# Optimization experiments

Hardware: AMD Instinct MI355X
Metric: run time of the kernel (lower is better)

The kernel has to match this reference:

```python
import jax, jax.numpy as jnp
import numpy as np

TAU = 2.0       # LIF time constant
VTH = 1.0       # V_THRESHOLD
ALPHA = 2.0     # ATan surrogate alpha (spikingjelly default)
SCALE = 0.125

@jax.custom_vjp
def spike(x):
    # Heaviside spike with ATan surrogate gradient
    return (x >= 0.0).astype(x.dtype)

def _spike_fwd(x):
    return (x >= 0.0).astype(x.dtype), x

def _spike_bwd(x, g):
    sg = (ALPHA / 2.0) / (1.0 + (jnp.pi / 2.0 * ALPHA * x) ** 2)
    return (g * sg,)

spike.defvjp(_spike_fwd, _spike_bwd)

def lif(x_seq):
    # multi-step LIF: v += (x - v)/tau; spike; hard reset (v_reset=0, detach_reset)
    def step(v, x):
        v = v + (x - v) / TAU
        s = spike(v - VTH)
        v = v * (1.0 - jax.lax.stop_gradient(s))
        return v, s
    _, s = jax.lax.scan(step, jnp.zeros_like(x_seq[0]), x_seq)
    return s

def conn_lif(x_seq, y_seq):
    # connecting LIF: membrane charged by conv output + identity shortcut
    def step(v, xy):
        x, y = xy
        v = v + ((x + y) - v) / TAU
        s = spike(v - VTH)
        v = v * (1.0 - jax.lax.stop_gradient(s))
        return v, s
    _, s = jax.lax.scan(step, jnp.zeros_like(x_seq[0]), (x_seq, y_seq))
    return s

def conv1x1(x, W, b):
    # x: [T,B,C,N]; 1x1 Conv1d == channel GEMM
    return jnp.einsum('tbcn,oc->tbon', x, W) + b[None, None, :, None]

def setup_inputs() -> dict:
    key = jax.random.key(0)
    T, B, C, H, W = 4, 16, 512, 32, 32
    ks = jax.random.split(key, 5)
    wscale = 1.0 / np.sqrt(C)
    inp = {
        'x': jax.random.normal(ks[0], (T, B, C, H, W), jnp.float32),
        'Wq': jax.random.normal(ks[1], (C, C), jnp.float32) * wscale,
        'bq': jnp.zeros((C,), jnp.float32),
        'Wk': jax.random.normal(ks[2], (C, C), jnp.float32) * wscale,
        'bk': jnp.zeros((C,), jnp.float32),
        'Wv': jax.random.normal(ks[3], (C, C), jnp.float32) * wscale,
        'bv': jnp.zeros((C,), jnp.float32),
        'Wp': jax.random.normal(ks[4], (C, C), jnp.float32) * wscale,
        'bp': jnp.zeros((C,), jnp.float32),
        'num_heads': 8,
    }
    return inp

def reference(x, Wq, bq, Wk, bk, Wv, bv, Wp, bp, num_heads):
    T, B, C, H, W = x.shape
    N = H * W
    h = num_heads
    d = C // h
    qkv_x = x.reshape(T, B, C, N)

    def to_heads(s):  # [T,B,C,N] -> [T,B,h,N,d]
        return s.reshape(T, B, h, d, N).transpose(0, 1, 2, 4, 3)

    q = to_heads(lif(conv1x1(qkv_x, Wq, bq)))
    k = to_heads(lif(conv1x1(qkv_x, Wk, bk)))
    v = to_heads(lif(conv1x1(qkv_x, Wv, bv)))

    kv = jnp.einsum('tbhnd,tbhne->tbhde', k, v)            # K^T V: [T,B,h,d,d]
    out = jnp.einsum('tbhnd,tbhde->tbhne', q, kv) * SCALE  # Q @ (K^T V)
    out = out.transpose(0, 1, 2, 4, 3).reshape(T, B, C, N)
    out = lif(out)                                          # attn_sn
    out = conv1x1(out, Wp, bp).reshape(T, B, C, H, W)       # proj_reparam
    out = conn_lif(out, x)                                  # proj_sn(out, x)
    return out
```

## Files before the change

kernel.cpp:

```cpp
#include <hip/hip_runtime.h>

#define T_ 4
#define B_ 16
#define C_ 512
#define N_ 1024
#define H_ 8
#define D_ 64
#define SPK_ELEMS (33554432ull)

typedef _Float16 half8v __attribute__((ext_vector_type(8)));
typedef _Float16 half4v __attribute__((ext_vector_type(4)));
typedef float f32x4 __attribute__((ext_vector_type(4)));

#define KV_OFF_N  100663296ull
#define WB_OFF_N  109051904ull
#define XS_OFF_N  113246208ull

#define QKV_INV_SCALE (1.0f / 8388608.0f)
#define PROJ_INV_SCALE (1.0f / 4096.0f)

#define GLD16(gp, loff) \
  __builtin_amdgcn_global_load_lds( \
      (const __attribute__((address_space(1))) void*)(gp), \
      (__attribute__((address_space(3))) void*)(lds + (loff)), 16, 0, 0)

__global__ __launch_bounds__(256) void convert_w(
    const float* __restrict__ w0, const float* __restrict__ w1,
    const float* __restrict__ w2, const float* __restrict__ w3,
    _Float16* __restrict__ wb)
{
  int idx = blockIdx.x * 256 + threadIdx.x;
  int p = idx >> 18, rem = idx & 262143;
  const float* src = (p == 0) ? w0 : (p == 1) ? w1 : (p == 2) ? w2 : w3;
  float v = src[rem] * 4096.0f;
  _Float16 h1 = (_Float16)v;
  float r1 = v - (float)h1;
  _Float16 h2 = (_Float16)r1;
  size_t base = ((size_t)(p * 2)) << 18;
  wb[base + rem] = h1;
  wb[base + 262144 + rem] = h2;
}

__global__ __launch_bounds__(256) void convert_x(
    const float* __restrict__ x, _Float16* __restrict__ xs)
{
  __shared__ float tile[32][33];
  const int tb = blockIdx.z;
  const int c0 = blockIdx.y * 32, n0 = blockIdx.x * 32;
  const int tx = threadIdx.x, ty = threadIdx.y;
  const float* src = x + ((size_t)tb * C_ + c0) * N_ + n0;
#pragma unroll
  for (int k = 0; k < 4; ++k)
    tile[ty + 8 * k][tx] = src[(size_t)(ty + 8 * k) * N_ + tx];
  __syncthreads();
#pragma unroll
  for (int k = 0; k < 4; ++k) {
    int r = ty + 8 * k;
    float v = tile[tx][r] * 2048.0f;
    _Float16 h1 = (_Float16)v;
    float r1 = v - (float)h1;
    _Float16 h2 = (_Float16)r1;
    size_t o = ((size_t)tb * N_ + n0 + r) * C_ + c0 + tx;
    xs[o] = h1;
    xs[o + 33554432ull] = h2;
  }
}

__global__ __launch_bounds__(256) void qkv_mfma(
    const _Float16* __restrict__ wb, const _Float16* __restrict__ xs,
    const float* __restrict__ bq, const float* __restrict__ bk,
    const float* __restrict__ bv, unsigned char* __restrict__ spikes_base)
{
  __shared__ __align__(16) char lds[32768];
  const int tid = threadIdx.x;
  const int lane = tid & 63, wave = tid >> 6;
  const int ln15 = lane & 15, lq = lane >> 4;
  const int ot = blockIdx.x & 3, p = blockIdx.x >> 2;
  const int ntb = blockIdx.y, b = blockIdx.z;
  const int o0 = ot * 128, n0 = ntb * 32;

  const _Float16* gsrc[8];
#pragma unroll
  for (int i = 0; i < 8; ++i) {
    int u = i * 256 + tid;
    if (u < 1024) {
      int s = u >> 9, rem = u & 511;
      int row = rem >> 2, pc = rem & 3;
      int lc = pc ^ ((row >> 1) & 3);
      gsrc[i] = wb + (((size_t)(p * 2 + s)) << 18) + (size_t)(o0 + row) * C_ + lc * 8;
    } else {
      int v = u - 1024;
      int s = v >> 9, rem = v & 511;
      int t = rem >> 7, rem2 = rem & 127;
      int row = rem2 >> 2, pc = rem2 & 3;
      int lc = pc ^ ((row >> 1) & 3);
      gsrc[i] = xs + ((size_t)s * 33554432ull) +
                ((size_t)((t * B_ + b) * N_ + n0 + row)) * C_ + lc * 8;
    }
  }

  f32x4 acc[T_][2][2];
#pragma unroll
  for (int t = 0; t < T_; ++t)
#pragma unroll
    for (int mt = 0; mt < 2; ++mt)
#pragma unroll
      for (int nt = 0; nt < 2; ++nt)
        acc[t][mt][nt] = (f32x4){0.f, 0.f, 0.f, 0.f};

  int offA[2][2], offB[2][2];
#pragma unroll
  for (int s = 0; s < 2; ++s) {
#pragma unroll
    for (int mt = 0; mt < 2; ++mt) {
      int r = wave * 32 + mt * 16 + ln15;
      offA[s][mt] = s * 8192 + r * 64 + ((lq ^ ((r >> 1) & 3)) << 4);
    }
#pragma unroll
    for (int nt = 0; nt < 2; ++nt) {
      int n = nt * 16 + ln15;
      offB[s][nt] = 16384 + s * 8192 + n * 64 + ((lq ^ ((n >> 1) & 3)) << 4);
    }
  }

  for (int kk = 0; kk < 16; ++kk) {
#pragma unroll
    for (int i = 0; i < 8; ++i)
      GLD16(gsrc[i], i * 4096 + (tid & 192) * 16);
    __syncthreads();

    half8v wa[2][2];
#pragma unroll
    for (int s = 0; s < 2; ++s)
#pragma unroll
      for (int mt = 0; mt < 2; ++mt)
        wa[s][mt] = *(const half8v*)&lds[offA[s][mt]];

#pragma unroll
    for (int t = 0; t < T_; ++t) {
      half8v xb[2][2];
#pragma unroll
      for (int s = 0; s < 2; ++s)
#pragma unroll
        for (int nt = 0; nt < 2; ++nt)
          xb[s][nt] = *(const half8v*)&lds[offB[s][nt] + t * 2048];
#pragma unroll
      for (int mt = 0; mt < 2; ++mt)
#pragma unroll
        for (int nt = 0; nt < 2; ++nt) {
          f32x4 a = acc[t][mt][nt];
          a = __builtin_amdgcn_mfma_f32_16x16x32_f16(wa[0][mt], xb[1][nt], a, 0, 0, 0);
          a = __builtin_amdgcn_mfma_f32_16x16x32_f16(wa[1][mt], xb[0][nt], a, 0, 0, 0);
          a = __builtin_amdgcn_mfma_f32_16x16x32_f16(wa[0][mt], xb[0][nt], a, 0, 0, 0);
          acc[t][mt][nt] = a;
        }
    }
    __syncthreads();
#pragma unroll
    for (int i = 0; i < 8; ++i) gsrc[i] += 32;
  }

  const float* bias = (p == 0) ? bq : (p == 1) ? bk : bv;
  if (p == 0) {
    unsigned char* spq = spikes_base;
#pragma unroll
    for (int mt = 0; mt < 2; ++mt) {
      int obase = o0 + wave * 32 + mt * 16 + lq * 4;
      float b4[4] = {bias[obase], bias[obase + 1], bias[obase + 2], bias[obase + 3]};
#pragma unroll
      for (int nt = 0; nt < 2; ++nt) {
        int n = n0 + nt * 16 + ln15;
        float vm[4] = {0.f, 0.f, 0.f, 0.f};
#pragma unroll
        for (int t = 0; t < T_; ++t) {
          unsigned char sj[4];
#pragma unroll
          for (int r = 0; r < 4; ++r) {
            float y = acc[t][mt][nt][r] * QKV_INV_SCALE + b4[r];
            float v = vm[r] + (y - vm[r]) * 0.5f;
            bool s = (v >= 1.0f);
            sj[r] = s ? 1 : 0;
            vm[r] = s ? 0.f : v;
          }
          *(uchar4*)&spq[((size_t)(t * B_ + b) * N_ + n) * C_ + obase] =
              make_uchar4(sj[0], sj[1], sj[2], sj[3]);
        }
      }
    }
  } else {
    unsigned char* sp = spikes_base + (size_t)p * SPK_ELEMS;
#pragma unroll
    for (int mt = 0; mt < 2; ++mt)
#pragma unroll
      for (int r = 0; r < 4; ++r) {
        int o = o0 + wave * 32 + mt * 16 + lq * 4 + r;
        float bo = bias[o];
#pragma unroll
        for (int nt = 0; nt < 2; ++nt) {
          int n = n0 + nt * 16 + ln15;
          float vmem = 0.f;
#pragma unroll
          for (int t = 0; t < T_; ++t) {
            float y = acc[t][mt][nt][r] * QKV_INV_SCALE + bo;
            float v = vmem + (y - vmem) * 0.5f;
            bool s = (v >= 1.0f);
            sp[((size_t)(t * B_ + b) * C_ + o) * N_ + n] = s ? 1 : 0;
            vmem = s ? 0.f : v;
          }
        }
      }
  }
}

__global__ __launch_bounds__(256) void kv_f16(
    const unsigned char* __restrict__ sk, const unsigned char* __restrict__ sv,
    float* __restrict__ kvout)
{
  __shared__ _Float16 Kf[64 * 264];
  __shared__ _Float16 Vf[64 * 264];
  const int tid = threadIdx.x;
  const int lane = tid & 63, wave = tid >> 6;
  const int ln15 = lane & 15, lq = lane >> 4;
  const int h = blockIdx.x, b = blockIdx.y, t = blockIdx.z;

  const unsigned char* kb = sk + ((size_t)(t * B_ + b) * C_ + h * D_) * N_;
  const unsigned char* vb = sv + ((size_t)(t * B_ + b) * C_ + h * D_) * N_;

  f32x4 acc[4];
#pragma unroll
  for (int et = 0; et < 4; ++et) acc[et] = (f32x4){0.f, 0.f, 0.f, 0.f};

  const int row = tid >> 2, seg = (tid & 3) * 64;

  for (int nc = 0; nc < N_; nc += 256) {
    const unsigned char* kr = kb + (size_t)row * N_ + nc + seg;
    const unsigned char* vr = vb + (size_t)row * N_ + nc + seg;
#pragma unroll
    for (int j = 0; j < 16; ++j) {
      unsigned wk = *(const unsigned*)(kr + j * 4);
      unsigned lo = ((wk & 0xFFu) | ((wk & 0xFF00u) << 8)) * 0x3C00u;
      unsigned hi = (((wk >> 16) & 0xFFu) | ((wk >> 8) & 0xFF0000u)) * 0x3C00u;
      *(uint2*)&Kf[row * 264 + seg + j * 4] = make_uint2(lo, hi);
      unsigned wv = *(const unsigned*)(vr + j * 4);
      unsigned lo2 = ((wv & 0xFFu) | ((wv & 0xFF00u) << 8)) * 0x3C00u;
      unsigned hi2 = (((wv >> 16) & 0xFFu) | ((wv >> 8) & 0xFF0000u)) * 0x3C00u;
      *(uint2*)&Vf[row * 264 + seg + j * 4] = make_uint2(lo2, hi2);
    }
    __syncthreads();
#pragma unroll
    for (int ks = 0; ks < 8; ++ks) {
      half8v a = *(const half8v*)&Kf[(wave * 16 + ln15) * 264 + ks * 32 + lq * 8];
#pragma unroll
      for (int et = 0; et < 4; ++et) {
        half8v bf = *(const half8v*)&Vf[(et * 16 + ln15) * 264 + ks * 32 + lq * 8];
        acc[et] = __builtin_amdgcn_mfma_f32_16x16x32_f16(a, bf, acc[et], 0, 0, 0);
      }
    }
    __syncthreads();
  }

  float* o = kvout + ((size_t)(t * B_ + b) * H_ + h) * (D_ * D_);
#pragma unroll
  for (int et = 0; et < 4; ++et)
#pragma unroll
    for (int r = 0; r < 4; ++r) {
      int d = wave * 16 + lq * 4 + r;
      int e = et * 16 + ln15;
      o[d * D_ + e] = acc[et][r];
    }
}

__global__ __launch_bounds__(256) void attn_mfma(
    const unsigned char* __restrict__ sq2, const float* __restrict__ kv,
    unsigned short* __restrict__ sa)
{
  __shared__ _Float16 Qs[128 * 72];
  __shared__ _Float16 KVT[64 * 72];
  const int tid = threadIdx.x;
  const int lane = tid & 63, wave = tid >> 6;
  const int ln15 = lane & 15, lq = lane >> 4;
  const int n0 = blockIdx.x * 128;
  const int h = blockIdx.y, b = blockIdx.z;

  f32x4 vm[8];
#pragma unroll
  for (int nt = 0; nt < 8; ++nt) vm[nt] = (f32x4){0.f, 0.f, 0.f, 0.f};

  for (int t = 0; t < T_; ++t) {
    __syncthreads();
    const float* kvb = kv + ((size_t)(t * B_ + b) * H_ + h) * (D_ * D_);
#pragma unroll
    for (int l = 0; l < 16; ++l) {
      int idx = l * 256 + tid;
      int e = idx & 63, d = idx >> 6;
      KVT[e * 72 + d] = (_Float16)kvb[d * 64 + e];
    }
    const unsigned char* qb = sq2 + ((size_t)(t * B_ + b) * N_ + n0) * C_ + h * D_;
#pragma unroll
    for (int l = 0; l < 8; ++l) {
      int idx = l * 256 + tid;
      int n = idx >> 4, d4 = (idx & 15) * 4;
      uchar4 qu = *(const uchar4*)&qb[(size_t)n * C_ + d4];
      half4v hv;
      hv.x = qu.x ? (_Float16)1.0f : (_Float16)0.0f;
      hv.y = qu.y ? (_Float16)1.0f : (_Float16)0.0f;
      hv.z = qu.z ? (_Float16)1.0f : (_Float16)0.0f;
      hv.w = qu.w ? (_Float16)1.0f : (_Float16)0.0f;
      *(half4v*)&Qs[n * 72 + d4] = hv;
    }
    __syncthreads();

    half8v af[2];
#pragma unroll
    for (int kk = 0; kk < 2; ++kk)
      af[kk] = *(const half8v*)&KVT[(wave * 16 + ln15) * 72 + kk * 32 + lq * 8];

#pragma unroll
    for (int nt = 0; nt < 8; ++nt) {
      f32x4 a = (f32x4){0.f, 0.f, 0.f, 0.f};
#pragma unroll
      for (int kk = 0; kk < 2; ++kk) {
        half8v bf = *(const half8v*)&Qs[(nt * 16 + ln15) * 72 + kk * 32 + lq * 8];
        a = __builtin_amdgcn_mfma_f32_16x16x32_f16(af[kk], bf, a, 0, 0, 0);
      }
      unsigned short sj[4];
#pragma unroll
      for (int r = 0; r < 4; ++r) {
        float y = a[r] * 0.125f;
        float v = vm[nt][r] + (y - vm[nt][r]) * 0.5f;
        bool s = (v >= 1.0f);
        sj[r] = s ? 0x3C00 : 0;
        vm[nt][r] = s ? 0.f : v;
      }
      int n = n0 + nt * 16 + ln15;
      int c0 = h * D_ + wave * 16 + lq * 4;
      *(ushort4*)&sa[((size_t)(t * B_ + b) * N_ + n) * C_ + c0] =
          make_ushort4(sj[0], sj[1], sj[2], sj[3]);
    }
  }
}

__global__ __launch_bounds__(256) void proj_mfma(
    const _Float16* __restrict__ wb, const _Float16* __restrict__ sa,
    const float* __restrict__ bp, const float* __restrict__ x,
    float* __restrict__ out)
{
  __shared__ __align__(16) char lds[24576];
  const int tid = threadIdx.x;
  const int lane = tid & 63, wave = tid >> 6;
  const int ln15 = lane & 15, lq = lane >> 4;
  const int ot = blockIdx.x, ntb = blockIdx.y, b = blockIdx.z;
  const int o0 = ot * 128, n0 = ntb * 32;

  const _Float16* gsrc[6];
#pragma unroll
  for (int i = 0; i < 6; ++i) {
    int u = i * 256 + tid;
    if (u < 1024) {
      int s = u >> 9, rem = u & 511;
      int row = rem >> 2, pc = rem & 3;
      int lc = pc ^ ((row >> 1) & 3);
      gsrc[i] = wb + (((size_t)(3 * 2 + s)) << 18) + (size_t)(o0 + row) * C_ + lc * 8;
    } else {
      int v = u - 1024;
      int t = v >> 7, rem2 = v & 127;
      int row = rem2 >> 2, pc = rem2 & 3;
      int lc = pc ^ ((row >> 1) & 3);
      gsrc[i] = sa + ((size_t)((t * B_ + b) * N_ + n0 + row)) * C_ + lc * 8;
    }
  }

  f32x4 acc[T_][2][2];
#pragma unroll
  for (int t = 0; t < T_; ++t)
#pragma unroll
    for (int mt = 0; mt < 2; ++mt)
#pragma unroll
      for (int nt = 0; nt < 2; ++nt)
        acc[t][mt][nt] = (f32x4){0.f, 0.f, 0.f, 0.f};

  int offA[2][2], offB[2];
#pragma unroll
  for (int s = 0; s < 2; ++s)
#pragma unroll
    for (int mt = 0; mt < 2; ++mt) {
      int r = wave * 32 + mt * 16 + ln15;
      offA[s][mt] = s * 8192 + r * 64 + ((lq ^ ((r >> 1) & 3)) << 4);
    }
#pragma unroll
  for (int nt = 0; nt < 2; ++nt) {
    int n = nt * 16 + ln15;
    offB[nt] = 16384 + n * 64 + ((lq ^ ((n >> 1) & 3)) << 4);
  }

  for (int kk = 0; kk < 16; ++kk) {
#pragma unroll
    for (int i = 0; i < 6; ++i)
      GLD16(gsrc[i], i * 4096 + (tid & 192) * 16);
    __syncthreads();

    half8v wa[2][2];
#pragma unroll
    for (int s = 0; s < 2; ++s)
#pragma unroll
      for (int mt = 0; mt < 2; ++mt)
        wa[s][mt] = *(const half8v*)&lds[offA[s][mt]];

#pragma unroll
    for (int t = 0; t < T_; ++t) {
      half8v xb[2];
#pragma unroll
      for (int nt = 0; nt < 2; ++nt)
        xb[nt] = *(const half8v*)&lds[offB[nt] + t * 2048];
#pragma unroll
      for (int mt = 0; mt < 2; ++mt)
#pragma unroll
        for (int nt = 0; nt < 2; ++nt) {
          f32x4 a = acc[t][mt][nt];
          a = __builtin_amdgcn_mfma_f32_16x16x32_f16(wa[1][mt], xb[nt], a, 0, 0, 0);
          a = __builtin_amdgcn_mfma_f32_16x16x32_f16(wa[0][mt], xb[nt], a, 0, 0, 0);
          acc[t][mt][nt] = a;
        }
    }
    __syncthreads();
#pragma unroll
    for (int i = 0; i < 6; ++i) gsrc[i] += 32;
  }

#pragma unroll
  for (int mt = 0; mt < 2; ++mt)
#pragma unroll
    for (int r = 0; r < 4; ++r) {
      int o = o0 + wave * 32 + mt * 16 + lq * 4 + r;
      float bo = bp[o];
#pragma unroll
      for (int nt = 0; nt < 2; ++nt) {
        int n = n0 + nt * 16 + ln15;
        float vmem = 0.f;
#pragma unroll
        for (int t = 0; t < T_; ++t) {
          size_t base = ((size_t)(t * B_ + b) * C_ + o) * N_ + n;
          float xv = x[base];
          float pv = acc[t][mt][nt][r] * PROJ_INV_SCALE + bo;
          float v = vmem + ((pv + xv) - vmem) * 0.5f;
          bool s = (v >= 1.0f);
          out[base] = s ? 1.0f : 0.0f;
          vmem = s ? 0.f : v;
        }
      }
    }
}

extern "C" void kernel_launch(void* const* d_in, const int* in_sizes, int n_in,
                              void* d_out, int out_size, void* d_ws, size_t ws_size,
                              hipStream_t stream)
{
  const float* x  = (const float*)d_in[0];
  const float* Wq = (const float*)d_in[1];
  const float* bq = (const float*)d_in[2];
  const float* Wk = (const float*)d_in[3];
  const float* bk = (const float*)d_in[4];
  const float* Wv = (const float*)d_in[5];
  const float* bv = (const float*)d_in[6];
  const float* Wp = (const float*)d_in[7];
  const float* bp = (const float*)d_in[8];
  (void)in_sizes; (void)n_in; (void)out_size; (void)ws_size;

  unsigned char* ws = (unsigned char*)d_ws;
  unsigned char* sq = ws;
  unsigned char* sk = ws + SPK_ELEMS;
  unsigned char* sv = ws + 2 * SPK_ELEMS;
  float* kvbuf = (float*)(ws + KV_OFF_N);
  _Float16* wb = (_Float16*)(ws + WB_OFF_N);
  _Float16* xs = (_Float16*)(ws + XS_OFF_N);
  unsigned short* sa = (unsigned short*)xs;
  float* out = (float*)d_out;

  convert_w<<<4096, 256, 0, stream>>>(Wq, Wk, Wv, Wp, wb);
  convert_x<<<dim3(32, 16, 64), dim3(32, 8), 0, stream>>>(x, xs);
  qkv_mfma<<<dim3(12, 32, 16), 256, 0, stream>>>(wb, xs, bq, bk, bv, ws);
  kv_f16<<<dim3(8, 16, 4), 256, 0, stream>>>(sk, sv, kvbuf);
  attn_mfma<<<dim3(8, 8, 16), 256, 0, stream>>>(sq, kvbuf, sa);
  proj_mfma<<<dim3(4, 32, 16), 256, 0, stream>>>(wb, (const _Float16*)sa, bp, x, out);
}
```

Baseline: 818.6 us.

## Double-buffer LDS tiles in QKV and projection GEMMs to overlap loads

```diff
diff --git a/kernel.cpp b/kernel.cpp
--- a/kernel.cpp
+++ b/kernel.cpp
@@ -71,7 +71,7 @@
     const float* __restrict__ bq, const float* __restrict__ bk,
     const float* __restrict__ bv, unsigned char* __restrict__ spikes_base)
 {
-  __shared__ __align__(16) char lds[32768];
+  __shared__ __align__(16) char lds[65536];
   const int tid = threadIdx.x;
   const int lane = tid & 63, wave = tid >> 6;
   const int ln15 = lane & 15, lq = lane >> 4;
@@ -123,19 +123,15 @@
     }
   }
 
-  for (int kk = 0; kk < 16; ++kk) {
-#pragma unroll
-    for (int i = 0; i < 8; ++i)
-      GLD16(gsrc[i], i * 4096 + (tid & 192) * 16);
-    __syncthreads();
-
+  auto compute = [&](int cur) {
     half8v wa[2][2];
 #pragma unroll
     for (int s = 0; s < 2; ++s)
 #pragma unroll
       for (int mt = 0; mt < 2; ++mt)
-        wa[s][mt] = *(const half8v*)&lds[offA[s][mt]];
-
+        wa[s][mt] = *(const half8v*)&lds[cur + offA[s][mt]];
+
+    __builtin_amdgcn_s_setprio(1);
 #pragma unroll
     for (int t = 0; t < T_; ++t) {
       half8v xb[2][2];
@@ -143,7 +139,7 @@
       for (int s = 0; s < 2; ++s)
 #pragma unroll
         for (int nt = 0; nt < 2; ++nt)
-          xb[s][nt] = *(const half8v*)&lds[offB[s][nt] + t * 2048];
+          xb[s][nt] = *(const half8v*)&lds[cur + offB[s][nt] + t * 2048];
 #pragma unroll
       for (int mt = 0; mt < 2; ++mt)
 #pragma unroll
@@ -155,10 +151,38 @@
           acc[t][mt][nt] = a;
         }
     }
-    __syncthreads();
+    __builtin_amdgcn_s_setprio(0);
+  };
+
+#pragma unroll
+  for (int i = 0; i < 8; ++i)
+    GLD16(gsrc[i], i * 4096 + (tid & 192) * 16);
+#pragma unroll
+  for (int i = 0; i < 8; ++i) gsrc[i] += 32;
+
+  for (int kk = 0; kk < 15; ++kk) {
+    const int cur = (kk & 1) << 15;
+    const int nxt = cur ^ 32768;
+#pragma unroll
+    for (int i = 0; i < 8; ++i)
+      GLD16(gsrc[i], nxt + i * 4096 + (tid & 192) * 16);
 #pragma unroll
     for (int i = 0; i < 8; ++i) gsrc[i] += 32;
-  }
+    __builtin_amdgcn_sched_barrier(0);
+    asm volatile("s_waitcnt vmcnt(8)" ::: "memory");
+    __builtin_amdgcn_s_barrier();
+    __builtin_amdgcn_sched_barrier(0);
+
+    compute(cur);
+
+    asm volatile("s_waitcnt lgkmcnt(0)" ::: "memory");
+    __builtin_amdgcn_sched_barrier(0);
+    __builtin_amdgcn_s_barrier();
+  }
+  asm volatile("s_waitcnt vmcnt(0)" ::: "memory");
+  __builtin_amdgcn_s_barrier();
+  __builtin_amdgcn_sched_barrier(0);
+  compute(32768);
 
   const float* bias = (p == 0) ? bq : (p == 1) ? bk : bv;
   if (p == 0) {
@@ -345,7 +369,7 @@
     const float* __restrict__ bp, const float* __restrict__ x,
     float* __restrict__ out)
 {
-  __shared__ __align__(16) char lds[24576];
+  __shared__ __align__(16) char lds[49152];
   const int tid = threadIdx.x;
   const int lane = tid & 63, wave = tid >> 6;
   const int ln15 = lane & 15, lq = lane >> 4;
@@ -393,25 +417,21 @@
     offB[nt] = 16384 + n * 64 + ((lq ^ ((n >> 1) & 3)) << 4);
   }
 
-  for (int kk = 0; kk < 16; ++kk) {
-#pragma unroll
-    for (int i = 0; i < 6; ++i)
-      GLD16(gsrc[i], i * 4096 + (tid & 192) * 16);
-    __syncthreads();
-
+  auto compute = [&](int cur) {
     half8v wa[2][2];
 #pragma unroll
     for (int s = 0; s < 2; ++s)
 #pragma unroll
       for (int mt = 0; mt < 2; ++mt)
-        wa[s][mt] = *(const half8v*)&lds[offA[s][mt]];
-
+        wa[s][mt] = *(const half8v*)&lds[cur + offA[s][mt]];
+
+    __builtin_amdgcn_s_setprio(1);
 #pragma unroll
     for (int t = 0; t < T_; ++t) {
       half8v xb[2];
 #pragma unroll
       for (int nt = 0; nt < 2; ++nt)
-        xb[nt] = *(const half8v*)&lds[offB[nt] + t * 2048];
+        xb[nt] = *(const half8v*)&lds[cur + offB[nt] + t * 2048];
 #pragma unroll
       for (int mt = 0; mt < 2; ++mt)
 #pragma unroll
@@ -422,10 +442,38 @@
           acc[t][mt][nt] = a;
         }
     }
-    __syncthreads();
+    __builtin_amdgcn_s_setprio(0);
+  };
+
+#pragma unroll
+  for (int i = 0; i < 6; ++i)
+    GLD16(gsrc[i], i * 4096 + (tid & 192) * 16);
+#pragma unroll
+  for (int i = 0; i < 6; ++i) gsrc[i] += 32;
+
+  for (int kk = 0; kk < 15; ++kk) {
+    const int cur = (kk & 1) * 24576;
+    const int nxt = 24576 - cur;
+#pragma unroll
+    for (int i = 0; i < 6; ++i)
+      GLD16(gsrc[i], nxt + i * 4096 + (tid & 192) * 16);
 #pragma unroll
     for (int i = 0; i < 6; ++i) gsrc[i] += 32;
-  }
+    __builtin_amdgcn_sched_barrier(0);
+    asm volatile("s_waitcnt vmcnt(6)" ::: "memory");
+    __builtin_amdgcn_s_barrier();
+    __builtin_amdgcn_sched_barrier(0);
+
+    compute(cur);
+
+    asm volatile("s_waitcnt lgkmcnt(0)" ::: "memory");
+    __builtin_amdgcn_sched_barrier(0);
+    __builtin_amdgcn_s_barrier();
+  }
+  asm volatile("s_waitcnt vmcnt(0)" ::: "memory");
+  __builtin_amdgcn_s_barrier();
+  __builtin_amdgcn_sched_barrier(0);
+  compute(24576);
 
 #pragma unroll
   for (int mt = 0; mt < 2; ++mt)
```

Measured after the change: 790.0 us. 1.04x faster.
